# Kernel optimization log

Hardware: AMD Instinct MI355X
Metric: run time of the kernel (lower is better)

## Reference

```python
import jax, jax.numpy as jnp
import numpy as np

D_MODEL = 1024
N_HEAD = 16
D_K = 64
D_V = 64
D_INNER = 4096
MAX_REL = 16
EPS = 1e-6


def _rel_index(length_q, length_k):
    # Shaw-style clipped relative distance matrix -> indices into embedding table
    dist = jnp.arange(length_k)[None, :] - jnp.arange(length_q)[:, None]
    return jnp.clip(dist, -MAX_REL, MAX_REL) + MAX_REL  # [Lq, Lk] in [0, 2*MAX_REL]


def _layer_norm(x, gamma, beta):
    mu = jnp.mean(x, axis=-1, keepdims=True)
    var = jnp.var(x, axis=-1, keepdims=True)
    return (x - mu) / jnp.sqrt(var + EPS) * gamma + beta


def setup_inputs() -> dict:
    key = jax.random.key(0)
    ks = jax.random.split(key, 16)
    B, L = 8, 1024
    s = 0.02
    inp = {
        "q": jax.random.normal(ks[0], (B, L, D_MODEL), jnp.float32),
        "k": jax.random.normal(ks[1], (B, L, D_MODEL), jnp.float32),
        "v": jax.random.normal(ks[2], (B, L, D_MODEL), jnp.float32),
        "wq": jax.random.normal(ks[3], (D_MODEL, D_MODEL), jnp.float32) * s,
        "bq": jnp.zeros((D_MODEL,), jnp.float32),
        "wk": jax.random.normal(ks[4], (D_MODEL, D_MODEL), jnp.float32) * s,
        "bk": jnp.zeros((D_MODEL,), jnp.float32),
        "wv": jax.random.normal(ks[5], (D_MODEL, D_MODEL), jnp.float32) * s,
        "bv": jnp.zeros((D_MODEL,), jnp.float32),
        "wfc": jax.random.normal(ks[6], (D_MODEL, D_MODEL), jnp.float32) * s,
        "bfc": jnp.zeros((D_MODEL,), jnp.float32),
        "w1": jax.random.normal(ks[7], (D_MODEL, D_INNER), jnp.float32) * s,
        "b1": jnp.zeros((D_INNER,), jnp.float32),
        "w2": jax.random.normal(ks[8], (D_INNER, D_MODEL), jnp.float32) * s,
        "b2": jnp.zeros((D_MODEL,), jnp.float32),
        "ln_g": jnp.ones((D_MODEL,), jnp.float32),
        "ln_b": jnp.zeros((D_MODEL,), jnp.float32),
        "rel_k": jax.random.normal(ks[9], (2 * MAX_REL + 1, D_K), jnp.float32) * s,
        "rel_v": jax.random.normal(ks[10], (2 * MAX_REL + 1, D_V), jnp.float32) * s,
    }
    return inp


def reference(q, k, v, wq, bq, wk, bk, wv, bv, wfc, bfc, w1, b1, w2, b2, ln_g, ln_b, rel_k, rel_v):
    B, Lq, _ = q.shape
    Lk = k.shape[1]
    residual = q

    Q = q @ wq + bq  # [B, Lq, D]
    K = k @ wk + bk
    V = v @ wv + bv

    Qh = Q.reshape(B, Lq, N_HEAD, D_K)  # [B, Lq, H, dk]
    Kh = K.reshape(B, Lk, N_HEAD, D_K)
    Vh = V.reshape(B, Lk, N_HEAD, D_V)

    # content-content scores
    attn1 = jnp.einsum("bqhd,bkhd->bhqk", Qh, Kh)
    # content-position scores (Shaw relative position)
    idx = _rel_index(Lq, Lk)  # [Lq, Lk]
    k2 = rel_k[idx]           # [Lq, Lk, dk]
    attn2 = jnp.einsum("bqhd,qkd->bhqk", Qh, k2)

    attn = (attn1 + attn2) / jnp.sqrt(jnp.float32(D_K))
    attn = jax.nn.softmax(attn, axis=-1)  # dropout = identity (eval)

    weight1 = jnp.einsum("bhqk,bkhd->bhqd", attn, Vh)
    v2 = rel_v[idx]  # [Lq, Lk, dv]
    weight2 = jnp.einsum("bhqk,qkd->bhqd", attn, v2)

    out = (weight1 + weight2).transpose(0, 2, 1, 3).reshape(B, Lq, N_HEAD * D_V)
    out = out @ wfc + bfc
    out = out + residual
    out = _layer_norm(out, ln_g, ln_b)

    residual = out
    out2 = jax.nn.relu(out @ w1 + b1) @ w2 + b2
    out = _layer_norm(out2 + residual, ln_g, ln_b)  # same LN params reused, as in source
    return out
```

## Files before the change

### kernel.cpp

```cpp
#include <hip/hip_runtime.h>
#include <stdint.h>


typedef __bf16 bf16x8 __attribute__((ext_vector_type(8)));
typedef float  f32x4  __attribute__((ext_vector_type(4)));

__device__ __forceinline__ unsigned short f2bf(float f) {
  union { float f; unsigned u; } x; x.f = f;
  unsigned r = x.u + 0x7fffu + ((x.u >> 16) & 1u);
  return (unsigned short)(r >> 16);
}
__device__ __forceinline__ float bf2f(unsigned short h) {
  union { unsigned u; float f; } x; x.u = ((unsigned)h) << 16; return x.f;
}

__device__ __forceinline__ void gload_lds16(
    const unsigned short* g,
    __attribute__((address_space(3))) unsigned int* l) {
  __builtin_amdgcn_global_load_lds(
      (const __attribute__((address_space(1))) unsigned int*)g, l, 16, 0, 0);
}

template<int EPI>
__global__ __launch_bounds__(256) void gemm_bt(
    const unsigned short* __restrict__ A,
    const unsigned short* __restrict__ Bt,
    const float* __restrict__ bias,
    void* __restrict__ Cout,
    int M, int N, int K)
{
  __shared__ __align__(16) unsigned short As[128 * 32];
  __shared__ __align__(16) unsigned short Bs[128 * 32];
  const int tid = threadIdx.x;
  const int lane = tid & 63, wv = tid >> 6;
  const int lq = lane >> 4, lm = lane & 15;
  const int wr = wv >> 1, wc = wv & 1;
  const int m0 = blockIdx.y * 128, n0 = blockIdx.x * 128;

  const unsigned short* ga0 = A  + (size_t)(m0 + (tid >> 2)) * K + (tid & 3) * 8;
  const unsigned short* gb0 = Bt + (size_t)(n0 + (tid >> 2)) * K + (tid & 3) * 8;
  const size_t rstep = (size_t)64 * K;

  __attribute__((address_space(3))) unsigned int* lA =
      (__attribute__((address_space(3))) unsigned int*)As + wv * 256;
  __attribute__((address_space(3))) unsigned int* lB =
      (__attribute__((address_space(3))) unsigned int*)Bs + wv * 256;

  const char* fa = (const char*)As + (wr * 64 + lm) * 64 + lq * 16;
  const char* fb = (const char*)Bs + (wc * 64 + lm) * 64 + lq * 16;

  f32x4 acc[4][4] = {};
  const int nk = K >> 5;
  for (int kt = 0; kt < nk; ++kt) {
    __syncthreads();
    gload_lds16(ga0,         lA);
    gload_lds16(ga0 + rstep, lA + 1024);
    gload_lds16(gb0,         lB);
    gload_lds16(gb0 + rstep, lB + 1024);
    ga0 += 32; gb0 += 32;
    __syncthreads();
    bf16x8 af[4], bfr[4];
    #pragma unroll
    for (int i = 0; i < 4; ++i) af[i]  = *(const bf16x8*)(fa + i * 16 * 64);
    #pragma unroll
    for (int j = 0; j < 4; ++j) bfr[j] = *(const bf16x8*)(fb + j * 16 * 64);
    #pragma unroll
    for (int i = 0; i < 4; ++i)
      #pragma unroll
      for (int j = 0; j < 4; ++j)
        acc[i][j] = __builtin_amdgcn_mfma_f32_16x16x32_bf16(af[i], bfr[j], acc[i][j], 0, 0, 0);
  }
  #pragma unroll
  for (int i = 0; i < 4; ++i) {
    #pragma unroll
    for (int j = 0; j < 4; ++j) {
      const int col = n0 + wc * 64 + j * 16 + lm;
      const float bv = bias[col];
      #pragma unroll
      for (int r = 0; r < 4; ++r) {
        const int row = m0 + wr * 64 + i * 16 + lq * 4 + r;
        float v = acc[i][j][r] + bv;
        if (EPI == 2) v = fmaxf(v, 0.0f);
        if (EPI == 1) ((float*)Cout)[(size_t)row * N + col] = v;
        else ((unsigned short*)Cout)[(size_t)row * N + col] = f2bf(v);
      }
    }
  }
}

__global__ __launch_bounds__(256) void tcast(
    const float* __restrict__ in, unsigned short* __restrict__ out, int R, int C)
{
  __shared__ float tile[32][33];
  const int tx = threadIdx.x & 31, ty = threadIdx.x >> 5;
  const int r0 = blockIdx.y * 32, c0 = blockIdx.x * 32;
  #pragma unroll
  for (int s = 0; s < 4; ++s)
    tile[ty + s * 8][tx] = in[(size_t)(r0 + ty + s * 8) * C + c0 + tx];
  __syncthreads();
  #pragma unroll
  for (int s = 0; s < 4; ++s)
    out[(size_t)(c0 + ty + s * 8) * R + r0 + tx] = f2bf(tile[tx][ty + s * 8]);
}

__global__ __launch_bounds__(256) void cast4(
    const float* __restrict__ in, unsigned short* __restrict__ out, int n)
{
  int i = (blockIdx.x * 256 + threadIdx.x) * 4;
  if (i < n) {
    float4 v = *(const float4*)(in + i);
    ushort4 o;
    o.x = f2bf(v.x); o.y = f2bf(v.y); o.z = f2bf(v.z); o.w = f2bf(v.w);
    *(ushort4*)(out + i) = o;
  }
}

__global__ __launch_bounds__(256) void vtrans(
    const unsigned short* __restrict__ VP, unsigned short* __restrict__ VPT)
{
  __shared__ unsigned short tile[64 * 66];
  const int pt = blockIdx.x, h = blockIdx.y, b = blockIdx.z;
  const int tid = threadIdx.x;
  const int p = tid >> 2, c0 = (tid & 3) * 16;
  const unsigned short* src = VP + (size_t)(b * 1024 + pt * 64 + p) * 1024 + h * 64 + c0;
  union { uint4 q; unsigned int u[4]; } t0, t1;
  t0.q = *(const uint4*)src;
  t1.q = *(const uint4*)(src + 8);
  #pragma unroll
  for (int e = 0; e < 4; ++e) {
    *(unsigned int*)&tile[p * 66 + c0 + e * 2]     = t0.u[e];
    *(unsigned int*)&tile[p * 66 + c0 + 8 + e * 2] = t1.u[e];
  }
  __syncthreads();
  const int d = tid >> 2, p0 = (tid & 3) * 16;
  union { uint4 q[2]; unsigned short s[16]; } ob;
  #pragma unroll
  for (int e = 0; e < 16; ++e) ob.s[e] = tile[(p0 + e) * 66 + d];
  unsigned short* dst = VPT + ((size_t)(h * 64 + d) * 8 + b) * 1024 + pt * 64 + p0;
  *(uint4*)dst       = ob.q[0];
  *(uint4*)(dst + 8) = ob.q[1];
}

__global__ __launch_bounds__(256, 3) void attn_flash(
    const unsigned short* __restrict__ Qp,
    const unsigned short* __restrict__ Kp,
    const unsigned short* __restrict__ VPT,
    const float* __restrict__ relk,
    const float* __restrict__ relv,
    unsigned short* __restrict__ ctx)
{
  const int qt = blockIdx.x, h = blockIdx.y, b = blockIdx.z;
  const int tid = threadIdx.x;
  const int lane = tid & 63, wv = tid >> 6;
  const int lq = lane >> 4, lm = lane & 15;

  __shared__ __align__(16) unsigned short Kt[64][72];
  __shared__ __align__(16) unsigned short Vt[64][72];
  __shared__ __align__(16) unsigned short Pt[64][72];
  __shared__ __align__(16) unsigned short relvT[64][32];
  __shared__ float qrel_s[64][33];
  __shared__ float Racc[64][33];

  const int tok0 = b * 1024 + qt * 64;

  for (int i = tid; i < 64 * 33; i += 256) {
    const int rr = i / 33, ss = i - rr * 33;
    Racc[rr][ss] = 0.0f;
  }
  for (int i = tid; i < 64 * 32; i += 256) {
    const int dd = i >> 5, ss = i & 31;
    relvT[dd][ss] = f2bf(relv[ss * 64 + dd]);
  }

  bf16x8 qf0, qf1;
  {
    const unsigned short* qg = Qp + (size_t)(tok0 + wv * 16 + lm) * 1024 + h * 64;
    qf0 = *(const bf16x8*)(qg + lq * 8);
    qf1 = *(const bf16x8*)(qg + 32 + lq * 8);
  }

  #pragma unroll
  for (int t = 0; t < 3; ++t) {
    const int bin = t * 16 + lm;
    union { bf16x8 v; unsigned short s[8]; } rk0, rk1;
    #pragma unroll
    for (int e = 0; e < 8; ++e) { rk0.s[e] = 0; rk1.s[e] = 0; }
    if (bin < 33) {
      const float* rp = relk + bin * 64 + lq * 8;
      #pragma unroll
      for (int e = 0; e < 8; ++e) {
        rk0.s[e] = f2bf(rp[e]);
        rk1.s[e] = f2bf(rp[32 + e]);
      }
    }
    f32x4 Sr = {};
    Sr = __builtin_amdgcn_mfma_f32_16x16x32_bf16(qf0, rk0.v, Sr, 0, 0, 0);
    Sr = __builtin_amdgcn_mfma_f32_16x16x32_bf16(qf1, rk1.v, Sr, 0, 0, 0);
    if (bin < 33) {
      #pragma unroll
      for (int r = 0; r < 4; ++r) qrel_s[wv * 16 + lq * 4 + r][bin] = Sr[r];
    }
  }
  __syncthreads();

  float e0f[4], e32f[4];
  #pragma unroll
  for (int r = 0; r < 4; ++r) {
    const int rowl = wv * 16 + lq * 4 + r;
    e0f[r]  = __expf(qrel_s[rowl][0]  * 0.125f);
    e32f[r] = __expf(qrel_s[rowl][32] * 0.125f);
  }

  f32x4 Oa[4] = {};
  float rsum[4] = {0, 0, 0, 0}, r0a[4] = {0, 0, 0, 0}, r32a[4] = {0, 0, 0, 0};

  const int srow = tid >> 2, scol = (tid & 3) * 16;
  const unsigned short* kg = Kp + (size_t)(b * 1024 + srow) * 1024 + h * 64 + scol;
  const unsigned short* vg = VPT + ((size_t)(h * 64 + srow) * 8 + b) * 1024 + scol;
  const int qa0 = qt * 64 + wv * 16;

  for (int kt = 0; kt < 16; ++kt) {
    __syncthreads();
    *(uint4*)&Kt[srow][scol]     = *(const uint4*)(kg);
    *(uint4*)&Kt[srow][scol + 8] = *(const uint4*)(kg + 8);
    *(uint4*)&Vt[srow][scol]     = *(const uint4*)(vg);
    *(uint4*)&Vt[srow][scol + 8] = *(const uint4*)(vg + 8);
    kg += 64 * 1024;
    vg += 64;
    __syncthreads();

    #pragma unroll
    for (int tj = 0; tj < 4; ++tj) {
      bf16x8 kf0 = *(const bf16x8*)(&Kt[tj * 16 + lm][lq * 8]);
      bf16x8 kf1 = *(const bf16x8*)(&Kt[tj * 16 + lm][32 + lq * 8]);
      f32x4 S = {};
      S = __builtin_amdgcn_mfma_f32_16x16x32_bf16(qf0, kf0, S, 0, 0, 0);
      S = __builtin_amdgcn_mfma_f32_16x16x32_bf16(qf1, kf1, S, 0, 0, 0);
      const int c0 = kt * 64 + tj * 16;
      if (c0 + 31 <= qa0) {
        #pragma unroll
        for (int r = 0; r < 4; ++r) {
          const float p = __expf(S[r] * 0.125f) * e0f[r];
          r0a[r] += p; rsum[r] += p;
          Pt[wv * 16 + lq * 4 + r][tj * 16 + lm] = f2bf(p);
        }
      } else if (c0 >= qa0 + 31) {
        #pragma unroll
        for (int r = 0; r < 4; ++r) {
          const float p = __expf(S[r] * 0.125f) * e32f[r];
          r32a[r] += p; rsum[r] += p;
          Pt[wv * 16 + lq * 4 + r][tj * 16 + lm] = f2bf(p);
        }
      } else {
        const int kpos = c0 + lm;
        #pragma unroll
        for (int r = 0; r < 4; ++r) {
          const int rowl = wv * 16 + lq * 4 + r;
          const int dist = kpos - (qt * 64 + rowl);
          const int bin = (dist < -16 ? 0 : (dist > 16 ? 32 : dist + 16));
          const float p = __expf((S[r] + qrel_s[rowl][bin]) * 0.125f);
          rsum[r] += p;
          if (bin == 0)       r0a[r]  += p;
          else if (bin == 32) r32a[r] += p;
          else Racc[rowl][bin] = p;
          Pt[rowl][tj * 16 + lm] = f2bf(p);
        }
      }
    }
    __syncthreads();
    #pragma unroll
    for (int dt = 0; dt < 4; ++dt) {
      #pragma unroll
      for (int kc = 0; kc < 2; ++kc) {
        bf16x8 pf = *(const bf16x8*)(&Pt[wv * 16 + lm][kc * 32 + lq * 8]);
        bf16x8 vf = *(const bf16x8*)(&Vt[dt * 16 + lm][kc * 32 + lq * 8]);
        Oa[dt] = __builtin_amdgcn_mfma_f32_16x16x32_bf16(pf, vf, Oa[dt], 0, 0, 0);
      }
    }
  }

  #pragma unroll
  for (int r = 0; r < 4; ++r) {
    #pragma unroll
    for (int off = 1; off < 16; off <<= 1) {
      rsum[r] += __shfl_xor(rsum[r], off, 64);
      r0a[r]  += __shfl_xor(r0a[r],  off, 64);
      r32a[r] += __shfl_xor(r32a[r], off, 64);
    }
  }
  if (lm == 0) {
    #pragma unroll
    for (int r = 0; r < 4; ++r) Racc[wv * 16 + lq * 4 + r][0] = r0a[r];
  }
  __syncthreads();
  for (int i = tid; i < 64 * 32; i += 256) {
    const int rr = i >> 5, cc = i & 31;
    Pt[rr][cc] = f2bf(Racc[rr][cc]);
  }
  __syncthreads();

  bf16x8 raf = *(const bf16x8*)(&Pt[wv * 16 + lm][lq * 8]);
  #pragma unroll
  for (int dt = 0; dt < 4; ++dt) {
    bf16x8 rvb = *(const bf16x8*)(&relvT[dt * 16 + lm][lq * 8]);
    f32x4 O2 = {};
    O2 = __builtin_amdgcn_mfma_f32_16x16x32_bf16(raf, rvb, O2, 0, 0, 0);
    const float rv32 = relv[32 * 64 + dt * 16 + lm];
    #pragma unroll
    for (int r = 0; r < 4; ++r) {
      const int rowl = wv * 16 + lq * 4 + r;
      const float v = (Oa[dt][r] + O2[r] + r32a[r] * rv32) / rsum[r];
      ctx[(size_t)(tok0 + rowl) * 1024 + h * 64 + dt * 16 + lm] = f2bf(v);
    }
  }
}

template<bool WB>
__global__ __launch_bounds__(256) void ln_res(
    const float* __restrict__ x, const float* __restrict__ res,
    const float* __restrict__ g, const float* __restrict__ bta,
    float* __restrict__ of, unsigned short* __restrict__ ob)
{
  const int row = blockIdx.x;
  const int tid = threadIdx.x;
  __shared__ float buf[1024];
  __shared__ float red[8];
  float s1 = 0.f, s2 = 0.f;
  for (int i = tid; i < 1024; i += 256) {
    const float v = x[(size_t)row * 1024 + i] + res[(size_t)row * 1024 + i];
    buf[i] = v; s1 += v; s2 += v * v;
  }
  #pragma unroll
  for (int off = 1; off < 64; off <<= 1) {
    s1 += __shfl_xor(s1, off, 64);
    s2 += __shfl_xor(s2, off, 64);
  }
  const int wv = tid >> 6;
  if ((tid & 63) == 0) { red[wv * 2] = s1; red[wv * 2 + 1] = s2; }
  __syncthreads();
  s1 = red[0] + red[2] + red[4] + red[6];
  s2 = red[1] + red[3] + red[5] + red[7];
  const float mean = s1 * (1.f / 1024.f);
  const float var = s2 * (1.f / 1024.f) - mean * mean;
  const float rstd = rsqrtf(var + 1e-6f);
  for (int i = tid; i < 1024; i += 256) {
    const float y = (buf[i] - mean) * rstd * g[i] + bta[i];
    of[(size_t)row * 1024 + i] = y;
    if (WB) ob[(size_t)row * 1024 + i] = f2bf(y);
  }
}

extern "C" void kernel_launch(void* const* d_in, const int* in_sizes, int n_in,
                              void* d_out, int out_size, void* d_ws, size_t ws_size,
                              hipStream_t stream) {
  (void)in_sizes; (void)n_in; (void)out_size; (void)ws_size;
  const float* q    = (const float*)d_in[0];
  const float* k    = (const float*)d_in[1];
  const float* v    = (const float*)d_in[2];
  const float* wq   = (const float*)d_in[3];
  const float* bq   = (const float*)d_in[4];
  const float* wk   = (const float*)d_in[5];
  const float* bk   = (const float*)d_in[6];
  const float* wv_  = (const float*)d_in[7];
  const float* bv   = (const float*)d_in[8];
  const float* wfc  = (const float*)d_in[9];
  const float* bfc  = (const float*)d_in[10];
  const float* w1   = (const float*)d_in[11];
  const float* b1   = (const float*)d_in[12];
  const float* w2   = (const float*)d_in[13];
  const float* b2   = (const float*)d_in[14];
  const float* ln_g = (const float*)d_in[15];
  const float* ln_b = (const float*)d_in[16];
  const float* rel_k = (const float*)d_in[17];
  const float* rel_v = (const float*)d_in[18];

  char* ws = (char*)d_ws;
  const size_t MB = 1ull << 20;
  unsigned short* WQT  = (unsigned short*)(ws + 0 * MB);
  unsigned short* WKT  = (unsigned short*)(ws + 2 * MB);
  unsigned short* WVT  = (unsigned short*)(ws + 4 * MB);
  unsigned short* WFCT = (unsigned short*)(ws + 6 * MB);
  unsigned short* W1T  = (unsigned short*)(ws + 8 * MB);
  unsigned short* W2T  = (unsigned short*)(ws + 16 * MB);
  unsigned short* QP   = (unsigned short*)(ws + 24 * MB);
  unsigned short* KP   = (unsigned short*)(ws + 40 * MB);
  unsigned short* VP   = (unsigned short*)(ws + 56 * MB);
  unsigned short* QBF  = (unsigned short*)(ws + 72 * MB);
  unsigned short* KBF  = (unsigned short*)(ws + 88 * MB);
  unsigned short* VBF  = (unsigned short*)(ws + 104 * MB);
  unsigned short* VPT  = QBF;
  unsigned short* CTX  = KBF;
  float*          OTMP = (float*)(ws + 104 * MB);
  float*          X1F  = (float*)(ws + 24 * MB);
  unsigned short* X1BF = VP;
  unsigned short* HBUF = (unsigned short*)(ws + 72 * MB);
  float*          Y2   = (float*)(ws + 136 * MB);

  const dim3 blk(256);
  const int NTOK = 8192;

  tcast<<<dim3(32, 32), blk, 0, stream>>>(wq, WQT, 1024, 1024);
  tcast<<<dim3(32, 32), blk, 0, stream>>>(wk, WKT, 1024, 1024);
  tcast<<<dim3(32, 32), blk, 0, stream>>>(wv_, WVT, 1024, 1024);
  tcast<<<dim3(32, 32), blk, 0, stream>>>(wfc, WFCT, 1024, 1024);
  tcast<<<dim3(128, 32), blk, 0, stream>>>(w1, W1T, 1024, 4096);
  tcast<<<dim3(32, 128), blk, 0, stream>>>(w2, W2T, 4096, 1024);
  cast4<<<8192, blk, 0, stream>>>(q, QBF, NTOK * 1024);
  cast4<<<8192, blk, 0, stream>>>(k, KBF, NTOK * 1024);
  cast4<<<8192, blk, 0, stream>>>(v, VBF, NTOK * 1024);

  gemm_bt<0><<<dim3(8, 64), blk, 0, stream>>>(QBF, WQT, bq, QP, NTOK, 1024, 1024);
  gemm_bt<0><<<dim3(8, 64), blk, 0, stream>>>(KBF, WKT, bk, KP, NTOK, 1024, 1024);
  gemm_bt<0><<<dim3(8, 64), blk, 0, stream>>>(VBF, WVT, bv, VP, NTOK, 1024, 1024);

  vtrans<<<dim3(16, 16, 8), blk, 0, stream>>>(VP, VPT);

  attn_flash<<<dim3(16, 16, 8), blk, 0, stream>>>(QP, KP, VPT, rel_k, rel_v, CTX);

  gemm_bt<1><<<dim3(8, 64), blk, 0, stream>>>(CTX, WFCT, bfc, OTMP, NTOK, 1024, 1024);
  ln_res<true><<<8192, blk, 0, stream>>>(OTMP, q, ln_g, ln_b, X1F, X1BF);
  gemm_bt<2><<<dim3(32, 64), blk, 0, stream>>>(X1BF, W1T, b1, HBUF, NTOK, 4096, 1024);
  gemm_bt<1><<<dim3(8, 64), blk, 0, stream>>>(HBUF, W2T, b2, Y2, NTOK, 1024, 4096);
  ln_res<false><<<8192, blk, 0, stream>>>(Y2, X1F, ln_g, ln_b, (float*)d_out, nullptr);
}
```

Before: 688.0 us.

## Swizzle GEMM blocks, use exp2 softmax with MFMA row sums, vectorize layernorm

Several unrelated changes land together. GEMM workgroup IDs are remapped in groups of eight, which is meant to improve L2 locality across XCDs. The attention softmax folds the scale and the log2e factor into an fma followed by a native exp2, drops the scalar row-sum accumulation and its shuffles, and computes row sums with an MFMA against a ones vector. The layernorm kernel is rewritten to use float4 loads and stores held in registers instead of a shared buffer. The f2bf helper now uses the compiler's bf16 conversion, and the MFMA row sum is taken over bf16-rounded probabilities, which slightly changes numerics.

```diff
diff --git a/kernel.cpp b/kernel.cpp
--- a/kernel.cpp
+++ b/kernel.cpp
@@ -6,9 +6,9 @@
 typedef float  f32x4  __attribute__((ext_vector_type(4)));
 
 __device__ __forceinline__ unsigned short f2bf(float f) {
-  union { float f; unsigned u; } x; x.f = f;
-  unsigned r = x.u + 0x7fffu + ((x.u >> 16) & 1u);
-  return (unsigned short)(r >> 16);
+  __bf16 h = (__bf16)f;
+  union { __bf16 h; unsigned short u; } x; x.h = h;
+  return x.u;
 }
 __device__ __forceinline__ float bf2f(unsigned short h) {
   union { unsigned u; float f; } x; x.u = ((unsigned)h) << 16; return x.f;
@@ -35,7 +35,12 @@
   const int lane = tid & 63, wv = tid >> 6;
   const int lq = lane >> 4, lm = lane & 15;
   const int wr = wv >> 1, wc = wv & 1;
-  const int m0 = blockIdx.y * 128, n0 = blockIdx.x * 128;
+
+  const int nx = gridDim.x;
+  const int nwg = nx * gridDim.y;
+  int bid = blockIdx.y * nx + blockIdx.x;
+  bid = (bid & 7) * (nwg >> 3) + (bid >> 3);
+  const int m0 = (bid / nx) * 128, n0 = (bid % nx) * 128;
 
   const unsigned short* ga0 = A  + (size_t)(m0 + (tid >> 2)) * K + (tid & 3) * 8;
   const unsigned short* gb0 = Bt + (size_t)(n0 + (tid >> 2)) * K + (tid & 3) * 8;
@@ -161,6 +166,8 @@
   __shared__ float qrel_s[64][33];
   __shared__ float Racc[64][33];
 
+  const float CE = 0.125f * 1.44269504088896340736f;
+
   const int tok0 = b * 1024 + qt * 64;
 
   for (int i = tid; i < 64 * 33; i += 256) {
@@ -198,21 +205,26 @@
     Sr = __builtin_amdgcn_mfma_f32_16x16x32_bf16(qf1, rk1.v, Sr, 0, 0, 0);
     if (bin < 33) {
       #pragma unroll
-      for (int r = 0; r < 4; ++r) qrel_s[wv * 16 + lq * 4 + r][bin] = Sr[r];
-    }
-  }
-  __syncthreads();
-
-  float e0f[4], e32f[4];
+      for (int r = 0; r < 4; ++r) qrel_s[wv * 16 + lq * 4 + r][bin] = Sr[r] * CE;
+    }
+  }
+  __syncthreads();
+
+  float q0a[4], q32a[4];
   #pragma unroll
   for (int r = 0; r < 4; ++r) {
     const int rowl = wv * 16 + lq * 4 + r;
-    e0f[r]  = __expf(qrel_s[rowl][0]  * 0.125f);
-    e32f[r] = __expf(qrel_s[rowl][32] * 0.125f);
-  }
+    q0a[r]  = qrel_s[rowl][0];
+    q32a[r] = qrel_s[rowl][32];
+  }
+
+  union { bf16x8 v; unsigned short s[8]; } one8;
+  #pragma unroll
+  for (int e = 0; e < 8; ++e) one8.s[e] = 0x3F80;
 
   f32x4 Oa[4] = {};
-  float rsum[4] = {0, 0, 0, 0}, r0a[4] = {0, 0, 0, 0}, r32a[4] = {0, 0, 0, 0};
+  f32x4 Rs = {};
+  float r0a[4] = {0, 0, 0, 0}, r32a[4] = {0, 0, 0, 0};
 
   const int srow = tid >> 2, scol = (tid & 3) * 16;
   const unsigned short* kg = Kp + (size_t)(b * 1024 + srow) * 1024 + h * 64 + scol;
@@ -240,15 +252,15 @@
       if (c0 + 31 <= qa0) {
         #pragma unroll
         for (int r = 0; r < 4; ++r) {
-          const float p = __expf(S[r] * 0.125f) * e0f[r];
-          r0a[r] += p; rsum[r] += p;
+          const float p = __builtin_amdgcn_exp2f(fmaf(S[r], CE, q0a[r]));
+          r0a[r] += p;
           Pt[wv * 16 + lq * 4 + r][tj * 16 + lm] = f2bf(p);
         }
       } else if (c0 >= qa0 + 31) {
         #pragma unroll
         for (int r = 0; r < 4; ++r) {
-          const float p = __expf(S[r] * 0.125f) * e32f[r];
-          r32a[r] += p; rsum[r] += p;
+          const float p = __builtin_amdgcn_exp2f(fmaf(S[r], CE, q32a[r]));
+          r32a[r] += p;
           Pt[wv * 16 + lq * 4 + r][tj * 16 + lm] = f2bf(p);
         }
       } else {
@@ -258,8 +270,7 @@
           const int rowl = wv * 16 + lq * 4 + r;
           const int dist = kpos - (qt * 64 + rowl);
           const int bin = (dist < -16 ? 0 : (dist > 16 ? 32 : dist + 16));
-          const float p = __expf((S[r] + qrel_s[rowl][bin]) * 0.125f);
-          rsum[r] += p;
+          const float p = __builtin_amdgcn_exp2f(fmaf(S[r], CE, qrel_s[rowl][bin]));
           if (bin == 0)       r0a[r]  += p;
           else if (bin == 32) r32a[r] += p;
           else Racc[rowl][bin] = p;
@@ -268,14 +279,17 @@
       }
     }
     __syncthreads();
+    const int prow = wv * 16 + lm;
+    bf16x8 pf0 = *(const bf16x8*)(&Pt[prow][lq * 8]);
+    bf16x8 pf1 = *(const bf16x8*)(&Pt[prow][32 + lq * 8]);
+    Rs = __builtin_amdgcn_mfma_f32_16x16x32_bf16(pf0, one8.v, Rs, 0, 0, 0);
+    Rs = __builtin_amdgcn_mfma_f32_16x16x32_bf16(pf1, one8.v, Rs, 0, 0, 0);
     #pragma unroll
     for (int dt = 0; dt < 4; ++dt) {
-      #pragma unroll
-      for (int kc = 0; kc < 2; ++kc) {
-        bf16x8 pf = *(const bf16x8*)(&Pt[wv * 16 + lm][kc * 32 + lq * 8]);
-        bf16x8 vf = *(const bf16x8*)(&Vt[dt * 16 + lm][kc * 32 + lq * 8]);
-        Oa[dt] = __builtin_amdgcn_mfma_f32_16x16x32_bf16(pf, vf, Oa[dt], 0, 0, 0);
-      }
+      bf16x8 vf0 = *(const bf16x8*)(&Vt[dt * 16 + lm][lq * 8]);
+      bf16x8 vf1 = *(const bf16x8*)(&Vt[dt * 16 + lm][32 + lq * 8]);
+      Oa[dt] = __builtin_amdgcn_mfma_f32_16x16x32_bf16(pf0, vf0, Oa[dt], 0, 0, 0);
+      Oa[dt] = __builtin_amdgcn_mfma_f32_16x16x32_bf16(pf1, vf1, Oa[dt], 0, 0, 0);
     }
   }
 
@@ -283,7 +297,6 @@
   for (int r = 0; r < 4; ++r) {
     #pragma unroll
     for (int off = 1; off < 16; off <<= 1) {
-      rsum[r] += __shfl_xor(rsum[r], off, 64);
       r0a[r]  += __shfl_xor(r0a[r],  off, 64);
       r32a[r] += __shfl_xor(r32a[r], off, 64);
     }
@@ -309,7 +322,7 @@
     #pragma unroll
     for (int r = 0; r < 4; ++r) {
       const int rowl = wv * 16 + lq * 4 + r;
-      const float v = (Oa[dt][r] + O2[r] + r32a[r] * rv32) / rsum[r];
+      const float v = (Oa[dt][r] + O2[r] + r32a[r] * rv32) / Rs[r];
       ctx[(size_t)(tok0 + rowl) * 1024 + h * 64 + dt * 16 + lm] = f2bf(v);
     }
   }
@@ -323,13 +336,13 @@
 {
   const int row = blockIdx.x;
   const int tid = threadIdx.x;
-  __shared__ float buf[1024];
   __shared__ float red[8];
-  float s1 = 0.f, s2 = 0.f;
-  for (int i = tid; i < 1024; i += 256) {
-    const float v = x[(size_t)row * 1024 + i] + res[(size_t)row * 1024 + i];
-    buf[i] = v; s1 += v; s2 += v * v;
-  }
+  const size_t base = (size_t)row * 1024 + tid * 4;
+  const float4 xv = *(const float4*)(x + base);
+  const float4 rv = *(const float4*)(res + base);
+  float v0 = xv.x + rv.x, v1 = xv.y + rv.y, v2 = xv.z + rv.z, v3 = xv.w + rv.w;
+  float s1 = v0 + v1 + v2 + v3;
+  float s2 = v0 * v0 + v1 * v1 + v2 * v2 + v3 * v3;
   #pragma unroll
   for (int off = 1; off < 64; off <<= 1) {
     s1 += __shfl_xor(s1, off, 64);
@@ -343,10 +356,18 @@
   const float mean = s1 * (1.f / 1024.f);
   const float var = s2 * (1.f / 1024.f) - mean * mean;
   const float rstd = rsqrtf(var + 1e-6f);
-  for (int i = tid; i < 1024; i += 256) {
-    const float y = (buf[i] - mean) * rstd * g[i] + bta[i];
-    of[(size_t)row * 1024 + i] = y;
-    if (WB) ob[(size_t)row * 1024 + i] = f2bf(y);
+  const float4 gv = *(const float4*)(g + tid * 4);
+  const float4 bv = *(const float4*)(bta + tid * 4);
+  float y0 = (v0 - mean) * rstd * gv.x + bv.x;
+  float y1 = (v1 - mean) * rstd * gv.y + bv.y;
+  float y2 = (v2 - mean) * rstd * gv.z + bv.z;
+  float y3 = (v3 - mean) * rstd * gv.w + bv.w;
+  float4 yo; yo.x = y0; yo.y = y1; yo.z = y2; yo.w = y3;
+  *(float4*)(of + base) = yo;
+  if (WB) {
+    ushort4 o;
+    o.x = f2bf(y0); o.y = f2bf(y1); o.z = f2bf(y2); o.w = f2bf(y3);
+    *(ushort4*)(ob + base) = o;
   }
 }
 
```

Result: faster. 659.8 us (-4.1%).
